# Optimization experiments

Hardware: AMD Instinct MI355X
Metric: run time of the kernel (lower is better)

Reference implementation:

```python
import jax, jax.numpy as jnp
import numpy as np
import math

DN = ('NCHW', 'OIHW', 'NCHW')

def conv(x, w, b, stride=1, pad=0):
    y = jax.lax.conv_general_dilated(x, w, (stride, stride), ((pad, pad), (pad, pad)), dimension_numbers=DN)
    return y + b[None, :, None, None]

def conv_t(x, w, b, stride=2, k=4, p=1):
    # torch ConvTranspose2d: weight (Cin, Cout, kH, kW). Equivalent fractionally-strided conv:
    w2 = jnp.transpose(w[:, :, ::-1, ::-1], (1, 0, 2, 3))  # -> (Cout, Cin, kH, kW), spatially flipped
    pp = k - 1 - p
    y = jax.lax.conv_general_dilated(x, w2, (1, 1), ((pp, pp), (pp, pp)), lhs_dilation=(stride, stride), dimension_numbers=DN)
    return y + b[None, :, None, None]

def res_stack(h, w1, b1, w2, b2):
    # w1: [L, rh, nh, 3, 3], w2: [L, nh, rh, 1, 1]
    for i in range(w1.shape[0]):
        t = conv(jax.nn.relu(h), w1[i], b1[i], 1, 1)
        t = conv(jax.nn.relu(t), w2[i], b2[i], 1, 0)
        h = h + t
    return jax.nn.relu(h)

def setup_inputs() -> dict:
    key = jax.random.key(0)
    ks = jax.random.split(key, 16)
    D, K = 64, 512
    limit = math.sqrt(3.0 / D)
    def w(k, shape, scale=0.05):
        return (jax.random.normal(k, shape, dtype=jnp.float32) * scale)
    return {
        'x': jax.random.normal(ks[0], (16, 3, 256, 256), dtype=jnp.float32),
        'enc_w0': w(ks[1], (64, 3, 4, 4)), 'enc_b0': jnp.zeros((64,), jnp.float32),
        'enc_w1': w(ks[2], (128, 64, 4, 4)), 'enc_b1': jnp.zeros((128,), jnp.float32),
        'enc_wf': w(ks[3], (128, 128, 3, 3)), 'enc_bf': jnp.zeros((128,), jnp.float32),
        'enc_res_w1': w(ks[4], (2, 32, 128, 3, 3)), 'enc_res_b1': jnp.zeros((2, 32), jnp.float32),
        'enc_res_w2': w(ks[5], (2, 128, 32, 1, 1)), 'enc_res_b2': jnp.zeros((2, 128), jnp.float32),
        'pre_w': w(ks[6], (64, 128, 1, 1)), 'pre_b': jnp.zeros((64,), jnp.float32),
        'codebook': jax.random.uniform(ks[7], (D, K), jnp.float32, -limit, limit),
        'dec_w': w(ks[8], (128, 64, 3, 3)), 'dec_b': jnp.zeros((128,), jnp.float32),
        'dec_res_w1': w(ks[9], (2, 32, 128, 3, 3)), 'dec_res_b1': jnp.zeros((2, 32), jnp.float32),
        'dec_res_w2': w(ks[10], (2, 128, 32, 1, 1)), 'dec_res_b2': jnp.zeros((2, 128), jnp.float32),
        'up_w0': w(ks[11], (128, 64, 4, 4)), 'up_b0': jnp.zeros((64,), jnp.float32),
        'up_w1': w(ks[12], (64, 3, 4, 4)), 'up_b1': jnp.zeros((3,), jnp.float32),
    }

def reference(x, enc_w0, enc_b0, enc_w1, enc_b1, enc_wf, enc_bf,
              enc_res_w1, enc_res_b1, enc_res_w2, enc_res_b2,
              pre_w, pre_b, codebook,
              dec_w, dec_b, dec_res_w1, dec_res_b1, dec_res_w2, dec_res_b2,
              up_w0, up_b0, up_w1, up_b1):
    # --- Encoder ---
    h = jax.nn.relu(conv(x, enc_w0, enc_b0, 2, 1))
    h = jax.nn.relu(conv(h, enc_w1, enc_b1, 2, 1))
    h = conv(h, enc_wf, enc_bf, 1, 1)
    h = res_stack(h, enc_res_w1, enc_res_b1, enc_res_w2, enc_res_b2)
    z = conv(h, pre_w, pre_b, 1, 0)  # [B, 64, 64, 64]
    # --- Vector quantizer (cdist + argmin + gather, straight-through) ---
    B, D, H, W = z.shape
    flat = jnp.transpose(z, (0, 2, 3, 1)).reshape(-1, D)  # [BHW, D]
    dist = (flat ** 2).sum(1, keepdims=True) - 2.0 * (flat @ codebook) + (codebook ** 2).sum(0)[None, :]
    idx = jnp.argmin(dist, axis=1)  # [BHW]
    q = codebook.T[idx].reshape(B, H, W, D).transpose(0, 3, 1, 2)
    zq = z + jax.lax.stop_gradient(q - z)  # straight-through estimator
    # --- Decoder ---
    h = conv(zq, dec_w, dec_b, 1, 1)
    h = res_stack(h, dec_res_w1, dec_res_b1, dec_res_w2, dec_res_b2)
    h = jax.nn.relu(conv_t(h, up_w0, up_b0, 2, 4, 1))
    x_recon = conv_t(h, up_w1, up_b1, 2, 4, 1)
    return x_recon
```

## Files before the change

### kernel.cpp

```cpp
#include <hip/hip_runtime.h>
#include <math.h>


#define DEV __device__ __forceinline__

DEV int rfl(int v) { return __builtin_amdgcn_readfirstlane(v); }

DEV void async_copy16(const float* g, float* l) {
  __builtin_amdgcn_global_load_lds(
      (const __attribute__((address_space(1))) void*)g,
      (__attribute__((address_space(3))) void*)l, 16, 0, 0);
}

typedef __attribute__((ext_vector_type(8))) _Float16 h16x8;
typedef __attribute__((ext_vector_type(4))) float f32x4;

DEV ushort f2h(float f) {
  _Float16 h = (_Float16)f;
  return __builtin_bit_cast(ushort, h);
}
DEV float h2f(ushort u) { return (float)__builtin_bit_cast(_Float16, u); }
DEV uint pk(ushort a, ushort b) { return (uint)a | ((uint)b << 16); }

template<int CIN, int COT>
__global__ __launch_bounds__(256) void prep_w3s(
    const float* __restrict__ w, ushort* __restrict__ wpk) {
  constexpr int nCh = CIN / 32, nM = COT / 16;
  const int t = blockIdx.x * 256 + threadIdx.x;
  if (t >= 9 * nCh * nM * 64) return;
  const int l = t & 63;
  const int m = (t >> 6) % nM;
  const int sid = t / (64 * nM);
  const int ch = sid / 9, khkw = sid % 9;
  const int co = m * 16 + (l & 15);
  const int k8 = (l >> 4) * 8;
  const int sw = (16 * l) ^ ((l & 4) ? 8 : 0);
  ushort* slab = wpk + (size_t)sid * (nM * 1024) + m * 1024;
#pragma unroll
  for (int i = 0; i < 8; i++) {
    const int ci = ch * 32 + k8 + i;
    const float v = w[((size_t)co * CIN + ci) * 9 + khkw];
    const ushort hi = f2h(v);
    slab[sw + i]       = hi;
    slab[(sw ^ 8) + i] = f2h((v - h2f(hi)) * 2048.0f);
  }
}

template<int CIN, int COT>
__global__ __launch_bounds__(256) void prep_w4s(
    const float* __restrict__ w, ushort* __restrict__ wpk) {
  const int t = blockIdx.x * 256 + threadIdx.x;
  if (t >= 16384) return;
  const int l = t & 63;
  const int m = (t >> 6) & 7;
  const int sid = t >> 9;
  const int step = sid >> 3, rr = (sid >> 2) & 1, kw = sid & 3;
  const int ch = step >> 1, h = step & 1;
  const int kh = 2 * h + rr;
  const int tap = kh * 4 + kw;
  const int co = m * 16 + (l & 15);
  const int k8 = (l >> 4) * 8;
  const int sw = (16 * l) ^ ((l & 4) ? 8 : 0);
  ushort* slab = wpk + (size_t)sid * 8192 + m * 1024;
#pragma unroll
  for (int i = 0; i < 8; i++) {
    const int ci = ch * 32 + k8 + i;
    const float v = w[((size_t)co * CIN + ci) * 16 + tap];
    const ushort hi = f2h(v);
    slab[sw + i]       = hi;
    slab[(sw ^ 8) + i] = f2h((v - h2f(hi)) * 2048.0f);
  }
}

template<int CIN, int COT>
__global__ __launch_bounds__(256) void prep_wt(
    const float* __restrict__ w, ushort* __restrict__ wpk) {
  constexpr int nCh = CIN / 32, nM = COT / 16;
  const int t = blockIdx.x * 256 + threadIdx.x;
  if (t >= 16 * nCh * nM * 64) return;
  const int l = t & 63;
  int q = t >> 6;
  const int m = q % nM;  q /= nM;
  const int ch = q % nCh; q /= nCh;
  const int kh = q >> 2, kw = q & 3;
  const int co = m * 16 + (l & 15);
  const int k8 = (l >> 4) * 8;
  ushort* o = wpk + (size_t)t * 16;
#pragma unroll
  for (int i = 0; i < 8; i++) {
    const int ci = ch * 32 + k8 + i;
    const float v = w[(((size_t)ci * COT + co) * 4 + kh) * 4 + kw];
    const ushort hi = f2h(v);
    o[i]     = hi;
    o[8 + i] = f2h((v - h2f(hi)) * 2048.0f);
  }
}

__global__ __launch_bounds__(256) void prep_cb(
    const float* __restrict__ cb, ushort* __restrict__ cbpk) {
  const int t = blockIdx.x * 256 + threadIdx.x;
  const int l = t & 63;
  const int m = (t >> 6) & 31;
  const int c = t >> 11;
  const int entry = m * 16 + (l & 15);
  ushort* o = cbpk + (size_t)t * 16;
#pragma unroll
  for (int i = 0; i < 8; i++) {
    const int d = c * 32 + (l >> 4) * 8 + i;
    const float v = cb[d * 512 + entry];
    const ushort hi = f2h(v);
    o[i]     = hi;
    o[8 + i] = f2h((v - h2f(hi)) * 2048.0f);
  }
}

__global__ __launch_bounds__(256) void cvt_cbn(
    const float* __restrict__ cb, float* __restrict__ cbn) {
  const int k = blockIdx.x * 256 + threadIdx.x;
  if (k >= 512) return;
  double s = 0.0;
  for (int d = 0; d < 64; d++) {
    const double c = (double)cb[d * 512 + k];
    s = fma(c, c, s);
  }
  cbn[k] = (float)s;
}

__global__ __launch_bounds__(256) void vq_mfma(
    const float* __restrict__ cb, const ushort* __restrict__ cbpk,
    const float* __restrict__ cbn, float* __restrict__ zq) {
  const int tid = threadIdx.x;
  const int l = tid & 63;
  const int w = rfl(tid >> 6);
  const int n = blockIdx.x >> 6, row = blockIdx.x & 63;
  float* zp = zq + (size_t)n * 262144 + row * 64;
  const int pos = w * 16 + (l & 15);

  h16x8 zh[2], zl[2];
#pragma unroll
  for (int c = 0; c < 2; c++) {
#pragma unroll
    for (int i = 0; i < 8; i++) {
      const int d = c * 32 + (l >> 4) * 8 + i;
      const float v = zp[(size_t)d * 4096 + pos];
      const _Float16 h = (_Float16)v;
      zh[c][i] = h;
      zl[c][i] = (_Float16)((v - (float)h) * 2048.0f);
    }
  }

  const float SCL = 1.0f / 2048.0f;
  float bestd = 1e30f;
  int best = 0;
  for (int grp = 0; grp < 4; grp++) {
    f32x4 aH[8], aM[8];
#pragma unroll
    for (int m = 0; m < 8; m++) {
      aH[m] = (f32x4){0.f, 0.f, 0.f, 0.f};
      aM[m] = (f32x4){0.f, 0.f, 0.f, 0.f};
    }
#pragma unroll
    for (int c = 0; c < 2; c++) {
#pragma unroll
      for (int m = 0; m < 8; m++) {
        const ushort* ap = cbpk + ((size_t)(c * 32 + grp * 8 + m) * 64 + l) * 16;
        const h16x8 ah = *(const h16x8*)ap;
        const h16x8 al = *(const h16x8*)(ap + 8);
        aH[m] = __builtin_amdgcn_mfma_f32_16x16x32_f16(ah, zh[c], aH[m], 0, 0, 0);
        aM[m] = __builtin_amdgcn_mfma_f32_16x16x32_f16(al, zh[c], aM[m], 0, 0, 0);
        aM[m] = __builtin_amdgcn_mfma_f32_16x16x32_f16(ah, zl[c], aM[m], 0, 0, 0);
      }
    }
#pragma unroll
    for (int m = 0; m < 8; m++) {
#pragma unroll
      for (int j = 0; j < 4; j++) {
        const int k = grp * 128 + m * 16 + ((l >> 4) << 2) + j;
        const float dd = aH[m][j] + aM[m][j] * SCL;
        const float dist = fmaf(-2.0f, dd, cbn[k]);
        if (dist < bestd) { bestd = dist; best = k; }
      }
    }
  }

#pragma unroll
  for (int off = 16; off <= 32; off <<= 1) {
    const float d2 = __shfl_xor(bestd, off, 64);
    const int i2 = __shfl_xor(best, off, 64);
    if (d2 < bestd || (d2 == bestd && i2 < best)) { bestd = d2; best = i2; }
  }

#pragma unroll
  for (int i = 0; i < 16; i++) {
    const int d = (l >> 4) * 16 + i;
    zp[(size_t)d * 4096 + pos] = cb[d * 512 + best];
  }
}

template<int CIN, int COT, bool RELU_OUT>
__global__ __launch_bounds__(256, 2) void conv4s2_mfma(
    const float* __restrict__ x, const ushort* __restrict__ wpk,
    const float* __restrict__ bias, float* __restrict__ y) {
  constexpr int nCh = CIN / 32, nM = COT / 16;
  constexpr int nStep = nCh * 2;
  constexpr int nTap = nStep * 8;
  __shared__ ushort act[2][2][2][66][40];
  __shared__ ushort wlds[2][8192];
  const int tid = threadIdx.x;
  const int l = tid & 63;
  const int wv = rfl(tid >> 6);
  const int ho = (blockIdx.x & 7) * 8 + (blockIdx.x >> 3);
  const int n = blockIdx.z;

  {
    uint* lp = (uint*)&act[0][0][0][0][0];
    for (int s = tid; s < 16 * 20; s += 256) {
      const int c = s / 20, w32 = s % 20;
      const int which = c & 1, rest = c >> 1;
      lp[(size_t)(rest * 66 + (which ? 65 : 0)) * 20 + w32] = 0;
    }
  }

  const float* xn = x + ((size_t)n * CIN) * 16384;

  float2 sreg[2][4][2];
  float rmask[2];
  auto LOADG = [&](int step) {
    const int ch = step >> 1, h = step & 1;
#pragma unroll
    for (int rr = 0; rr < 2; rr++) {
      const int ir = 2 * ho - 1 + 2 * h + rr;
      const bool ok = (ir >= 0) && (ir < 128);
      const int irc = ok ? ir : 0;
      rmask[rr] = ok ? 1.0f : 0.0f;
#pragma unroll
      for (int cc = 0; cc < 4; cc++) {
        const int ci0 = ch * 32 + cc * 8 + wv * 2;
        sreg[rr][cc][0] = *(const float2*)(xn + (size_t)ci0 * 16384 + irc * 128 + 2 * l);
        sreg[rr][cc][1] = *(const float2*)(xn + (size_t)(ci0 + 1) * 16384 + irc * 128 + 2 * l);
      }
    }
  };
  auto WRITE = [&]() {
    uint* base = (uint*)&act[0][0][0][0][0];
#pragma unroll
    for (int rr = 0; rr < 2; rr++) {
#pragma unroll
      for (int cc = 0; cc < 4; cc++) {
        const float e0 = sreg[rr][cc][0].x * rmask[rr], o0 = sreg[rr][cc][0].y * rmask[rr];
        const float e1 = sreg[rr][cc][1].x * rmask[rr], o1 = sreg[rr][cc][1].y * rmask[rr];
        const ushort he0 = f2h(e0), ho_0 = f2h(o0);
        const ushort he1 = f2h(e1), ho_1 = f2h(o1);
        const ushort le0 = f2h((e0 - h2f(he0)) * 2048.0f);
        const ushort lo0 = f2h((o0 - h2f(ho_0)) * 2048.0f);
        const ushort le1 = f2h((e1 - h2f(he1)) * 2048.0f);
        const ushort lo1 = f2h((o1 - h2f(ho_1)) * 2048.0f);
        const int u = cc * 4 + wv;
        const size_t sl20 = (size_t)(l + 1) * 20 + u;
        base[(size_t)((0 * 2 + rr) * 2 + 0) * 1320 + sl20] = pk(he0, he1);
        base[(size_t)((0 * 2 + rr) * 2 + 1) * 1320 + sl20] = pk(ho_0, ho_1);
        base[(size_t)((1 * 2 + rr) * 2 + 0) * 1320 + sl20] = pk(le0, le1);
        base[(size_t)((1 * 2 + rr) * 2 + 1) * 1320 + sl20] = pk(lo0, lo1);
      }
    }
  };
  auto STAGEW = [&](int t, int buf) {
    const ushort* src = wpk + (size_t)t * 8192;
    ushort* dst = &wlds[buf][0];
#pragma unroll
    for (int j = 0; j < 4; j++)
      async_copy16((const float*)(src + (j * 256 + tid) * 8),
                   (float*)(dst + (j * 256 + tid) * 8));
  };

  f32x4 accH[nM], accM[nM];
#pragma unroll
  for (int m = 0; m < nM; m++) {
    const int co = m * 16 + ((l >> 4) << 2);
    accH[m] = (f32x4){bias[co], bias[co + 1], bias[co + 2], bias[co + 3]};
    accM[m] = (f32x4){0.f, 0.f, 0.f, 0.f};
  }

  const int pb = wv * 16;
  const int sw = (16 * l) ^ ((l & 4) ? 8 : 0);
  STAGEW(0, 0);
  LOADG(0);
  int tcnt = 0;
  for (int step = 0; step < nStep; step++) {
    __syncthreads();
    WRITE();
    __syncthreads();
#pragma unroll
    for (int rr = 0; rr < 2; rr++) {
#pragma unroll
      for (int kw = 0; kw < 4; kw++) {
        if (!(rr == 0 && kw == 0)) __syncthreads();
        if (tcnt + 1 < nTap) STAGEW(tcnt + 1, (tcnt + 1) & 1);
        if (rr == 0 && kw == 0 && step + 1 < nStep) LOADG(step + 1);
        const ushort* wb = &wlds[tcnt & 1][0];
        const int eo = (kw == 0 || kw == 2) ? 1 : 0;
        const int sh = (kw == 0) ? 0 : (kw == 3) ? 2 : 1;
        const int sl = pb + (l & 15) + sh;
        const h16x8 bh = *(const h16x8*)(&act[0][rr][eo][sl][(l >> 4) * 8]);
        const h16x8 bl = *(const h16x8*)(&act[1][rr][eo][sl][(l >> 4) * 8]);
#pragma unroll
        for (int m = 0; m < nM; m++) {
          const h16x8 ah = *(const h16x8*)(wb + m * 1024 + sw);
          const h16x8 al = *(const h16x8*)(wb + m * 1024 + (sw ^ 8));
          accH[m] = __builtin_amdgcn_mfma_f32_16x16x32_f16(ah, bh, accH[m], 0, 0, 0);
          accM[m] = __builtin_amdgcn_mfma_f32_16x16x32_f16(al, bh, accM[m], 0, 0, 0);
          accM[m] = __builtin_amdgcn_mfma_f32_16x16x32_f16(ah, bl, accM[m], 0, 0, 0);
        }
        tcnt++;
      }
    }
  }

  const float SCL = 1.0f / 2048.0f;
  const int pos = pb + (l & 15);
  const int r4 = (l >> 4) << 2;
#pragma unroll
  for (int m = 0; m < nM; m++) {
    const int co = m * 16 + r4;
    float* yp = y + (((size_t)(n * COT + co)) * 64 + ho) * 64 + pos;
#pragma unroll
    for (int j = 0; j < 4; j++) {
      float v = accH[m][j] + accM[m][j] * SCL;
      if (RELU_OUT) v = fmaxf(v, 0.f);
      yp[(size_t)j * 4096] = v;
    }
  }
}

template<int CIN, int COT, bool RELU_IN>
__global__ __launch_bounds__(256, 2) void conv3_mfma(
    const float* __restrict__ x, const ushort* __restrict__ wpk,
    const float* __restrict__ bias, float* __restrict__ y) {
  constexpr int nCh = CIN / 32, nM = COT / 16;
  constexpr int nTap = nCh * 9;
  __shared__ ushort act[2][3 * 66 * 40];
  __shared__ ushort wlds[2][nM * 1024];
  const int tid = threadIdx.x;
  const int l = tid & 63;
  const int wv = rfl(tid >> 6);
  const int r = blockIdx.x;
  const int n = blockIdx.z;

  {
    uint* lp = (uint*)&act[0][0];
    for (int s = tid; s < 12 * 20; s += 256) {
      const int c = s / 20, w32 = s % 20;
      const int which = c & 1;
      const int rowrel = (c >> 1) % 3;
      const int plane  = (c >> 1) / 3;
      lp[(size_t)(plane * 198 + rowrel * 66 + (which ? 65 : 0)) * 20 + w32] = 0;
    }
  }

  const float* xn = x + ((size_t)n * CIN) * 4096;

  float sreg[3][4][2];
  auto LOADG = [&](int ch) {
#pragma unroll
    for (int rr = 0; rr < 3; rr++) {
      const int ir = r - 1 + rr;
      const bool ok = (ir >= 0) && (ir < 64);
#pragma unroll
      for (int cc = 0; cc < 4; cc++) {
        const int ci0 = ch * 32 + cc * 8 + wv * 2;
        sreg[rr][cc][0] = ok ? xn[((size_t)ci0 * 64 + ir) * 64 + l] : 0.f;
        sreg[rr][cc][1] = ok ? xn[((size_t)(ci0 + 1) * 64 + ir) * 64 + l] : 0.f;
      }
    }
  };
  auto WRITE = [&]() {
    uint* ph = (uint*)&act[0][0];
    uint* pl = (uint*)&act[1][0];
#pragma unroll
    for (int rr = 0; rr < 3; rr++) {
#pragma unroll
      for (int cc = 0; cc < 4; cc++) {
        float v0 = sreg[rr][cc][0], v1 = sreg[rr][cc][1];
        if (RELU_IN) { v0 = fmaxf(v0, 0.f); v1 = fmaxf(v1, 0.f); }
        const ushort h0 = f2h(v0), h1 = f2h(v1);
        const ushort m0 = f2h((v0 - h2f(h0)) * 2048.0f);
        const ushort m1 = f2h((v1 - h2f(h1)) * 2048.0f);
        const int idx = (rr * 66 + (l + 1)) * 20 + cc * 4 + wv;
        ph[idx] = (uint)h0 | ((uint)h1 << 16);
        pl[idx] = (uint)m0 | ((uint)m1 << 16);
      }
    }
  };
  auto STAGEW = [&](int t, int buf) {
    const ushort* src = wpk + (size_t)t * (nM * 1024);
    ushort* dst = &wlds[buf][0];
#pragma unroll
    for (int j = 0; j < nM / 2; j++)
      async_copy16((const float*)(src + (j * 256 + tid) * 8),
                   (float*)(dst + (j * 256 + tid) * 8));
  };

  f32x4 accH[nM], accM[nM];
#pragma unroll
  for (int m = 0; m < nM; m++) {
    const int co = m * 16 + ((l >> 4) << 2);
    accH[m] = (f32x4){bias[co], bias[co + 1], bias[co + 2], bias[co + 3]};
    accM[m] = (f32x4){0.f, 0.f, 0.f, 0.f};
  }

  const int pb = wv * 16;
  const int sw = (16 * l) ^ ((l & 4) ? 8 : 0);
  STAGEW(0, 0);
  LOADG(0);
  int tcnt = 0;
  for (int ch = 0; ch < nCh; ch++) {
    __syncthreads();
    WRITE();
    __syncthreads();
#pragma unroll
    for (int kh = 0; kh < 3; kh++) {
#pragma unroll
      for (int kw = 0; kw < 3; kw++) {
        if (!(kh == 0 && kw == 0)) __syncthreads();
        if (tcnt + 1 < nTap) STAGEW(tcnt + 1, (tcnt + 1) & 1);
        if (kh == 0 && kw == 0 && ch + 1 < nCh) LOADG(ch + 1);
        const ushort* wb = &wlds[tcnt & 1][0];
        const int slot = kh * 66 + pb + (l & 15) + kw;
        const h16x8 bh = *(const h16x8*)(&act[0][0] + slot * 40 + (l >> 4) * 8);
        const h16x8 bl = *(const h16x8*)(&act[1][0] + slot * 40 + (l >> 4) * 8);
#pragma unroll
        for (int m = 0; m < nM; m++) {
          const h16x8 ah = *(const h16x8*)(wb + m * 1024 + sw);
          const h16x8 al = *(const h16x8*)(wb + m * 1024 + (sw ^ 8));
          accH[m] = __builtin_amdgcn_mfma_f32_16x16x32_f16(ah, bh, accH[m], 0, 0, 0);
          accM[m] = __builtin_amdgcn_mfma_f32_16x16x32_f16(al, bh, accM[m], 0, 0, 0);
          accM[m] = __builtin_amdgcn_mfma_f32_16x16x32_f16(ah, bl, accM[m], 0, 0, 0);
        }
        tcnt++;
      }
    }
  }

  const float SCL = 1.0f / 2048.0f;
  const int pos = pb + (l & 15);
  const int r4 = (l >> 4) << 2;
#pragma unroll
  for (int m = 0; m < nM; m++) {
    const int co = m * 16 + r4;
    float* yp = y + (((size_t)(n * COT + co)) * 64 + r) * 64 + pos;
#pragma unroll
    for (int j = 0; j < 4; j++)
      yp[(size_t)j * 4096] = accH[m][j] + accM[m][j] * SCL;
  }
}

template<int CIN, int COT, bool RELU_OUT>
__global__ __launch_bounds__(256, 2) void convt_mfma(
    const float* __restrict__ x, const ushort* __restrict__ wpk,
    const float* __restrict__ bias, float* __restrict__ y) {
  constexpr int nCh = CIN / 32, nM = COT / 16;
  __shared__ ushort lds[2][2][3 * 66 * 40];
  const int tid = threadIdx.x;
  const int l = tid & 63;
  const int wv = rfl(tid >> 6);
  const int a = blockIdx.x;
  const int n = blockIdx.z;

  {
    uint* lp = (uint*)&lds[0][0][0];
    for (int s = tid; s < 24 * 20; s += 256) {
      const int slot = s / 20, w32 = s % 20;
      const int which = slot & 1;
      const int rowrel = (slot >> 1) % 3;
      const int plane  = ((slot >> 1) / 3) & 1;
      const int buf    = (slot >> 1) / 6;
      lp[(size_t)((buf * 2 + plane) * 198 + rowrel * 66 + (which ? 65 : 0)) * 20 + w32] = 0;
    }
  }

  const float* xn = x + ((size_t)n * CIN) * 4096;

  float sreg[3][4][2];
  auto LOADG = [&](int ch) {
#pragma unroll
    for (int rr = 0; rr < 3; rr++) {
      const int ir = a - 1 + rr;
      const bool ok = (ir >= 0) && (ir < 64);
#pragma unroll
      for (int cc = 0; cc < 4; cc++) {
        const int ci0 = ch * 32 + cc * 8 + wv * 2;
        sreg[rr][cc][0] = ok ? xn[((size_t)ci0 * 64 + ir) * 64 + l] : 0.f;
        sreg[rr][cc][1] = ok ? xn[((size_t)(ci0 + 1) * 64 + ir) * 64 + l] : 0.f;
      }
    }
  };
  auto WRITE = [&](int buf) {
    uint* ph = (uint*)&lds[buf][0][0];
    uint* pl = (uint*)&lds[buf][1][0];
#pragma unroll
    for (int rr = 0; rr < 3; rr++) {
#pragma unroll
      for (int cc = 0; cc < 4; cc++) {
        const float v0 = sreg[rr][cc][0], v1 = sreg[rr][cc][1];
        const ushort h0 = f2h(v0), h1 = f2h(v1);
        const ushort m0 = f2h((v0 - h2f(h0)) * 2048.0f);
        const ushort m1 = f2h((v1 - h2f(h1)) * 2048.0f);
        const int idx = (rr * 66 + (l + 1)) * 20 + cc * 4 + wv;
        ph[idx] = (uint)h0 | ((uint)h1 << 16);
        pl[idx] = (uint)m0 | ((uint)m1 << 16);
      }
    }
  };

  f32x4 aH[4][nM], aM[4][nM];
#pragma unroll
  for (int m = 0; m < nM; m++) {
    const int co = m * 16 + ((l >> 4) << 2);
    const f32x4 b4 = (f32x4){bias[co], bias[co + 1], bias[co + 2], bias[co + 3]};
#pragma unroll
    for (int o = 0; o < 4; o++) { aH[o][m] = b4; aM[o][m] = (f32x4){0.f,0.f,0.f,0.f}; }
  }

  const int pb = wv * 16;
  LOADG(0); WRITE(0);
  if (nCh > 1) LOADG(1);
  int cur = 0;

#define CT_APPLY(OIDX, KH, KW) {                                              \
    const ushort* wp_ = wpk + (((size_t)((KH) * 4 + (KW)) * nCh + ch) * nM * 64 + l) * 16; \
    _Pragma("unroll")                                                         \
    for (int m = 0; m < nM; m++) {                                            \
      const h16x8 ah = *(const h16x8*)(wp_ + (size_t)m * 1024);               \
      const h16x8 al = *(const h16x8*)(wp_ + (size_t)m * 1024 + 8);           \
      aH[OIDX][m] = __builtin_amdgcn_mfma_f32_16x16x32_f16(ah, bh, aH[OIDX][m], 0, 0, 0); \
      aM[OIDX][m] = __builtin_amdgcn_mfma_f32_16x16x32_f16(al, bh, aM[OIDX][m], 0, 0, 0); \
      aM[OIDX][m] = __builtin_amdgcn_mfma_f32_16x16x32_f16(ah, bl, aM[OIDX][m], 0, 0, 0); \
    }}
#define CT_FRAG(RR, DD)                                                       \
    const int slot = (RR) * 66 + pb + (l & 15) + 1 + (DD);                    \
    const h16x8 bh = *(const h16x8*)(base_h + slot * 40 + (l >> 4) * 8);      \
    const h16x8 bl = *(const h16x8*)(base_l + slot * 40 + (l >> 4) * 8);

  for (int ch = 0; ch < nCh; ch++) {
    __syncthreads();
    const ushort* base_h = &lds[cur][0][0];
    const ushort* base_l = &lds[cur][1][0];
    { CT_FRAG(0, -1) CT_APPLY(0, 3, 3) }
    { CT_FRAG(0,  0) CT_APPLY(0, 3, 1) CT_APPLY(1, 3, 2) }
    { CT_FRAG(0, +1) CT_APPLY(1, 3, 0) }
    { CT_FRAG(1, -1) CT_APPLY(0, 1, 3) CT_APPLY(2, 2, 3) }
    { CT_FRAG(1,  0) CT_APPLY(0, 1, 1) CT_APPLY(1, 1, 2) CT_APPLY(2, 2, 1) CT_APPLY(3, 2, 2) }
    { CT_FRAG(1, +1) CT_APPLY(1, 1, 0) CT_APPLY(3, 2, 0) }
    { CT_FRAG(2, -1) CT_APPLY(2, 0, 3) }
    { CT_FRAG(2,  0) CT_APPLY(2, 0, 1) CT_APPLY(3, 0, 2) }
    { CT_FRAG(2, +1) CT_APPLY(3, 0, 0) }
    if (ch + 1 < nCh) {
      WRITE(cur ^ 1);
      if (ch + 2 < nCh) LOADG(ch + 2);
    }
    cur ^= 1;
  }
#undef CT_APPLY
#undef CT_FRAG

  const float SCL = 1.0f / 2048.0f;
  const int b = pb + (l & 15);
  const int oh0 = 2 * a;
  const int r4 = (l >> 4) << 2;
#pragma unroll
  for (int m = 0; m < nM; m++) {
    const int co = m * 16 + r4;
#pragma unroll
    for (int j = 0; j < 4; j++) {
      float v0e = aH[0][m][j] + aM[0][m][j] * SCL;
      float v0o = aH[1][m][j] + aM[1][m][j] * SCL;
      float v1e = aH[2][m][j] + aM[2][m][j] * SCL;
      float v1o = aH[3][m][j] + aM[3][m][j] * SCL;
      if (RELU_OUT) {
        v0e = fmaxf(v0e, 0.f); v0o = fmaxf(v0o, 0.f);
        v1e = fmaxf(v1e, 0.f); v1o = fmaxf(v1o, 0.f);
      }
      float* row0 = y + (((size_t)(n * COT + co + j)) * 128 + oh0) * 128;
      ((float2*)row0)[b] = make_float2(v0e, v0o);
      ((float2*)(row0 + 128))[b] = make_float2(v1e, v1o);
    }
  }
}

template<int CIN, int COT, bool RELU_OUT, int OW>
__global__ __launch_bounds__(256) void conv4s2_row(
    const float* __restrict__ x, const float* __restrict__ w,
    const float* __restrict__ bias, float* __restrict__ y,
    int Hout, int Cout) {
  const int Win = OW * 2, Hin = Hout * 2;
  const int t = blockIdx.x * 256 + threadIdx.x;
  const int wo = t & (OW - 1);
  const int ho = rfl(t / OW);
  const int co0 = blockIdx.y * COT, n = blockIdx.z;

  float acc[COT];
#pragma unroll
  for (int u = 0; u < COT; u++) acc[u] = bias[co0 + u];

  const int iw0 = 2 * wo - 1;
  const int cA = iw0 < 0 ? 0 : iw0;
  const bool mA = iw0 >= 0;
  const int cD = (iw0 + 3 < Win) ? iw0 + 3 : Win - 1;
  const bool mD = iw0 + 3 < Win;

  for (int ci = 0; ci < CIN; ci++) {
    const float* xp = x + ((size_t)(n * CIN + ci)) * Hin * Win;
    const float* wp = w + ((size_t)(co0 * CIN + ci)) * 16;
#pragma unroll
    for (int kh = 0; kh < 4; kh++) {
      const int ih = 2 * ho - 1 + kh;
      if (ih >= 0 && ih < Hin) {
        const float* row = xp + (size_t)ih * Win;
        float x0 = row[cA];      x0 = mA ? x0 : 0.f;
        float x1 = row[iw0 + 1];
        float x2 = row[iw0 + 2];
        float x3 = row[cD];      x3 = mD ? x3 : 0.f;
#pragma unroll
        for (int u = 0; u < COT; u++) {
          const float* wr = wp + u * CIN * 16 + kh * 4;
          acc[u] = fmaf(x0, wr[0], acc[u]);
          acc[u] = fmaf(x1, wr[1], acc[u]);
          acc[u] = fmaf(x2, wr[2], acc[u]);
          acc[u] = fmaf(x3, wr[3], acc[u]);
        }
      }
    }
  }
#pragma unroll
  for (int u = 0; u < COT; u++) {
    float v = acc[u];
    if (RELU_OUT) v = fmaxf(v, 0.f);
    y[(((size_t)(n * Cout + co0 + u)) * Hout + ho) * OW + wo] = v;
  }
}

template<int CIN, int COT, bool RELU_IN, bool ACCUM, bool RELU_OUT>
__global__ __launch_bounds__(256) void conv1x1_v4(
    const float* __restrict__ x, const float* __restrict__ w,
    const float* __restrict__ bias, float* __restrict__ y,
    int HW, int Cout) {
  const int p = (blockIdx.x * 256 + threadIdx.x) * 4;
  const int co0 = blockIdx.y * COT, n = blockIdx.z;

  float4 acc[COT];
#pragma unroll
  for (int u = 0; u < COT; u++) {
    const float b = bias[co0 + u];
    acc[u] = make_float4(b, b, b, b);
  }
  for (int ci = 0; ci < CIN; ci++) {
    float4 xv = *(const float4*)&x[((size_t)(n * CIN + ci)) * HW + p];
    if (RELU_IN) {
      xv.x = fmaxf(xv.x, 0.f); xv.y = fmaxf(xv.y, 0.f);
      xv.z = fmaxf(xv.z, 0.f); xv.w = fmaxf(xv.w, 0.f);
    }
#pragma unroll
    for (int u = 0; u < COT; u++) {
      const float wv = w[(co0 + u) * CIN + ci];
      acc[u].x = fmaf(xv.x, wv, acc[u].x);
      acc[u].y = fmaf(xv.y, wv, acc[u].y);
      acc[u].z = fmaf(xv.z, wv, acc[u].z);
      acc[u].w = fmaf(xv.w, wv, acc[u].w);
    }
  }
#pragma unroll
  for (int u = 0; u < COT; u++) {
    float4* yp = (float4*)&y[((size_t)(n * Cout + co0 + u)) * HW + p];
    float4 r = acc[u];
    if (ACCUM) {
      float4 h = *yp;
      r.x += h.x; r.y += h.y; r.z += h.z; r.w += h.w;
    }
    if (RELU_OUT) {
      r.x = fmaxf(r.x, 0.f); r.y = fmaxf(r.y, 0.f);
      r.z = fmaxf(r.z, 0.f); r.w = fmaxf(r.w, 0.f);
    }
    *yp = r;
  }
}

template<int CIN, int COT, bool RELU_IN, bool RELU_OUT, int WH>
__global__ __launch_bounds__(256) void convt_row(
    const float* __restrict__ x, const float* __restrict__ w,
    const float* __restrict__ bias, float* __restrict__ y,
    int Hin, int Cout) {
  const int Hout = Hin * 2;
  const int t = blockIdx.x * 256 + threadIdx.x;
  const int a = t & (WH - 1);
  const int oh = rfl(t / WH);
  const int co0 = blockIdx.y * COT, n = blockIdx.z;

  float acc0[COT], acc1[COT];
#pragma unroll
  for (int u = 0; u < COT; u++) { acc0[u] = bias[co0 + u]; acc1[u] = bias[co0 + u]; }

  const int cm = a > 0 ? a - 1 : 0;
  const bool mm = a > 0;
  const int cp = a < WH - 1 ? a + 1 : WH - 1;
  const bool mp = a < WH - 1;

  const int kh0 = (oh + 1) & 1;
#pragma unroll
  for (int dh = 0; dh < 2; dh++) {
    const int kh = kh0 + 2 * dh;
    const int ih = (oh + 1 - kh) >> 1;
    if (ih >= 0 && ih < Hin) {
      for (int ci = 0; ci < CIN; ci++) {
        const float* row = x + (((size_t)(n * CIN + ci)) * Hin + ih) * WH;
        float x0  = row[a];
        float xm1 = row[cm];  xm1 = mm ? xm1 : 0.f;
        float xp1 = row[cp];  xp1 = mp ? xp1 : 0.f;
        if (RELU_IN) {
          x0 = fmaxf(x0, 0.f); xm1 = fmaxf(xm1, 0.f); xp1 = fmaxf(xp1, 0.f);
        }
        const float* wp = w + ((size_t)(ci * Cout + co0)) * 16 + kh * 4;
#pragma unroll
        for (int u = 0; u < COT; u++) {
          const float* wr = wp + u * 16;
          acc0[u] = fmaf(x0,  wr[1], acc0[u]);
          acc0[u] = fmaf(xm1, wr[3], acc0[u]);
          acc1[u] = fmaf(xp1, wr[0], acc1[u]);
          acc1[u] = fmaf(x0,  wr[2], acc1[u]);
        }
      }
    }
  }
#pragma unroll
  for (int u = 0; u < COT; u++) {
    float v0 = acc0[u], v1 = acc1[u];
    if (RELU_OUT) { v0 = fmaxf(v0, 0.f); v1 = fmaxf(v1, 0.f); }
    float* row = y + (((size_t)(n * Cout + co0 + u)) * Hout + oh) * (2 * WH);
    ((float2*)row)[a] = make_float2(v0, v1);
  }
}

extern "C" void kernel_launch(void* const* d_in, const int* in_sizes, int n_in,
                              void* d_out, int out_size, void* d_ws, size_t ws_size,
                              hipStream_t stream) {
  const float* x          = (const float*)d_in[0];
  const float* enc_w0     = (const float*)d_in[1];
  const float* enc_b0     = (const float*)d_in[2];
  const float* enc_w1     = (const float*)d_in[3];
  const float* enc_b1     = (const float*)d_in[4];
  const float* enc_wf     = (const float*)d_in[5];
  const float* enc_bf     = (const float*)d_in[6];
  const float* enc_res_w1 = (const float*)d_in[7];
  const float* enc_res_b1 = (const float*)d_in[8];
  const float* enc_res_w2 = (const float*)d_in[9];
  const float* enc_res_b2 = (const float*)d_in[10];
  const float* pre_w      = (const float*)d_in[11];
  const float* pre_b      = (const float*)d_in[12];
  const float* codebook   = (const float*)d_in[13];
  const float* dec_w      = (const float*)d_in[14];
  const float* dec_b      = (const float*)d_in[15];
  const float* dec_res_w1 = (const float*)d_in[16];
  const float* dec_res_b1 = (const float*)d_in[17];
  const float* dec_res_w2 = (const float*)d_in[18];
  const float* dec_res_b2 = (const float*)d_in[19];
  const float* up_w0      = (const float*)d_in[20];
  const float* up_b0      = (const float*)d_in[21];
  const float* up_w1      = (const float*)d_in[22];
  const float* up_b1      = (const float*)d_in[23];
  float* out = (float*)d_out;

  float* A = (float*)d_ws;
  float* B = A + 16777216;
  float* C = B + 8388608;
  ushort* wpkF  = (ushort*)(A + 8388608);
  ushort* wpkEa = wpkF  + 294912;
  ushort* wpkEb = wpkEa + 73728;
  ushort* wpkD  = wpkEb + 73728;
  ushort* wpkDa = wpkD  + 147456;
  ushort* wpkDb = wpkDa + 73728;
  ushort* cbpk  = wpkDb + 73728;
  float*  cbn   = (float*)(cbpk + 131072);
  ushort* wpk1  = (ushort*)C;
  ushort* wpkT  = wpk1 + 262144;

  const dim3 blk(256);
  const int N = 16;

  prep_w4s<64, 128><<<dim3(64), blk, 0, stream>>>(enc_w1, wpk1);

  conv4s2_row<3, 16, true, 128><<<dim3(64, 4, N), blk, 0, stream>>>(
      x, enc_w0, enc_b0, A, 128, 64);
  conv4s2_mfma<64, 128, true><<<dim3(64, 1, N), blk, 0, stream>>>(
      A, wpk1, enc_b1, B);

  prep_w3s<128, 128><<<dim3(72), blk, 0, stream>>>(enc_wf, wpkF);
  prep_w3s<128, 32><<<dim3(18), blk, 0, stream>>>(enc_res_w1, wpkEa);
  prep_w3s<128, 32><<<dim3(18), blk, 0, stream>>>(
      enc_res_w1 + (size_t)32 * 128 * 9, wpkEb);
  prep_w3s<64, 128><<<dim3(36), blk, 0, stream>>>(dec_w, wpkD);
  prep_w3s<128, 32><<<dim3(18), blk, 0, stream>>>(dec_res_w1, wpkDa);
  prep_w3s<128, 32><<<dim3(18), blk, 0, stream>>>(
      dec_res_w1 + (size_t)32 * 128 * 9, wpkDb);
  prep_cb<<<dim3(16), blk, 0, stream>>>(codebook, cbpk);
  cvt_cbn<<<dim3(2), blk, 0, stream>>>(codebook, cbn);

  conv3_mfma<128, 128, false><<<dim3(64, 1, N), blk, 0, stream>>>(
      B, wpkF, enc_bf, C);
  conv3_mfma<128, 32, true><<<dim3(64, 1, N), blk, 0, stream>>>(
      C, wpkEa, enc_res_b1, A);
  conv1x1_v4<32, 8, true, true, false><<<dim3(4, 16, N), blk, 0, stream>>>(
      A, enc_res_w2, enc_res_b2, C, 4096, 128);
  conv3_mfma<128, 32, true><<<dim3(64, 1, N), blk, 0, stream>>>(
      C, wpkEb, enc_res_b1 + 32, A);
  conv1x1_v4<32, 8, true, true, true><<<dim3(4, 16, N), blk, 0, stream>>>(
      A, enc_res_w2 + (size_t)128 * 32, enc_res_b2 + 128, C, 4096, 128);
  conv1x1_v4<128, 8, false, false, false><<<dim3(4, 8, N), blk, 0, stream>>>(
      C, pre_w, pre_b, A, 4096, 64);

  prep_wt<128, 64><<<dim3(64), blk, 0, stream>>>(up_w0, wpkT);

  vq_mfma<<<dim3(1024), blk, 0, stream>>>(codebook, cbpk, cbn, A);

  conv3_mfma<64, 128, false><<<dim3(64, 1, N), blk, 0, stream>>>(
      A, wpkD, dec_b, B);
  conv3_mfma<128, 32, true><<<dim3(64, 1, N), blk, 0, stream>>>(
      B, wpkDa, dec_res_b1, A);
  conv1x1_v4<32, 8, true, true, false><<<dim3(4, 16, N), blk, 0, stream>>>(
      A, dec_res_w2, dec_res_b2, B, 4096, 128);
  conv3_mfma<128, 32, true><<<dim3(64, 1, N), blk, 0, stream>>>(
      B, wpkDb, dec_res_b1 + 32, A);
  conv1x1_v4<32, 8, true, true, true><<<dim3(4, 16, N), blk, 0, stream>>>(
      A, dec_res_w2 + (size_t)128 * 32, dec_res_b2 + 128, B, 4096, 128);
  convt_mfma<128, 64, true><<<dim3(64, 1, N), blk, 0, stream>>>(
      B, wpkT, up_b0, A);
  convt_row<64, 3, false, false, 128><<<dim3(128, 1, N), blk, 0, stream>>>(
      A, up_w1, up_b1, out, 128, 3);
}
```

Before: 813.8 us.

## Stage transposed-conv weights through LDS with async double-buffered copies

The transposed-conv kernel now streams each tap's weight slab into double-buffered LDS using async global-to-LDS copies, instead of every wave reading weights straight from global memory. The weight prep kernel is changed to emit slabs in the order the taps are consumed, with a swizzled layout to reduce LDS bank conflicts. The activation buffer drops from double to single buffering to make room. The cost is a __syncthreads before every tap apply plus extra barriers around the activation write, which may serialize the MFMA work.

Measured after the change: 777.7 us. 1.05x faster.

```diff
diff --git a/kernel.cpp b/kernel.cpp
--- a/kernel.cpp
+++ b/kernel.cpp
@@ -73,26 +73,29 @@
 }
 
 template<int CIN, int COT>
-__global__ __launch_bounds__(256) void prep_wt(
+__global__ __launch_bounds__(256) void prep_wts(
     const float* __restrict__ w, ushort* __restrict__ wpk) {
   constexpr int nCh = CIN / 32, nM = COT / 16;
   const int t = blockIdx.x * 256 + threadIdx.x;
   if (t >= 16 * nCh * nM * 64) return;
   const int l = t & 63;
-  int q = t >> 6;
-  const int m = q % nM;  q /= nM;
-  const int ch = q % nCh; q /= nCh;
-  const int kh = q >> 2, kw = q & 3;
+  const int m = (t >> 6) % nM;
+  const int sid = t / (64 * nM);
+  const int ch = sid >> 4, idx = sid & 15;
+  const int ord[16] = {15, 13, 14, 12, 7, 11, 5, 6, 9, 10, 4, 8, 3, 1, 2, 0};
+  const int tap = ord[idx];
+  const int kh = tap >> 2, kw = tap & 3;
   const int co = m * 16 + (l & 15);
   const int k8 = (l >> 4) * 8;
-  ushort* o = wpk + (size_t)t * 16;
+  const int sw = (16 * l) ^ ((l & 4) ? 8 : 0);
+  ushort* slab = wpk + (size_t)sid * (nM * 1024) + m * 1024;
 #pragma unroll
   for (int i = 0; i < 8; i++) {
     const int ci = ch * 32 + k8 + i;
     const float v = w[(((size_t)ci * COT + co) * 4 + kh) * 4 + kw];
     const ushort hi = f2h(v);
-    o[i]     = hi;
-    o[8 + i] = f2h((v - h2f(hi)) * 2048.0f);
+    slab[sw + i]       = hi;
+    slab[(sw ^ 8) + i] = f2h((v - h2f(hi)) * 2048.0f);
   }
 }
 
@@ -459,7 +462,9 @@
     const float* __restrict__ x, const ushort* __restrict__ wpk,
     const float* __restrict__ bias, float* __restrict__ y) {
   constexpr int nCh = CIN / 32, nM = COT / 16;
-  __shared__ ushort lds[2][2][3 * 66 * 40];
+  constexpr int nTap = nCh * 16;
+  __shared__ ushort act[2][3 * 66 * 40];
+  __shared__ ushort wlds[2][nM * 1024];
   const int tid = threadIdx.x;
   const int l = tid & 63;
   const int wv = rfl(tid >> 6);
@@ -467,14 +472,13 @@
   const int n = blockIdx.z;
 
   {
-    uint* lp = (uint*)&lds[0][0][0];
-    for (int s = tid; s < 24 * 20; s += 256) {
-      const int slot = s / 20, w32 = s % 20;
-      const int which = slot & 1;
-      const int rowrel = (slot >> 1) % 3;
-      const int plane  = ((slot >> 1) / 3) & 1;
-      const int buf    = (slot >> 1) / 6;
-      lp[(size_t)((buf * 2 + plane) * 198 + rowrel * 66 + (which ? 65 : 0)) * 20 + w32] = 0;
+    uint* lp = (uint*)&act[0][0];
+    for (int s = tid; s < 12 * 20; s += 256) {
+      const int c = s / 20, w32 = s % 20;
+      const int which = c & 1;
+      const int rowrel = (c >> 1) % 3;
+      const int plane  = (c >> 1) / 3;
+      lp[(size_t)(plane * 198 + rowrel * 66 + (which ? 65 : 0)) * 20 + w32] = 0;
     }
   }
 
@@ -494,9 +498,9 @@
       }
     }
   };
-  auto WRITE = [&](int buf) {
-    uint* ph = (uint*)&lds[buf][0][0];
-    uint* pl = (uint*)&lds[buf][1][0];
+  auto WRITE = [&]() {
+    uint* ph = (uint*)&act[0][0];
+    uint* pl = (uint*)&act[1][0];
 #pragma unroll
     for (int rr = 0; rr < 3; rr++) {
 #pragma unroll
@@ -511,6 +515,14 @@
       }
     }
   };
+  auto STAGEW = [&](int t, int buf) {
+    const ushort* src = wpk + (size_t)t * (nM * 1024);
+    ushort* dst = &wlds[buf][0];
+#pragma unroll
+    for (int j = 0; j < nM / 2; j++)
+      async_copy16((const float*)(src + (j * 256 + tid) * 8),
+                   (float*)(dst + (j * 256 + tid) * 8));
+  };
 
   f32x4 aH[4][nM], aM[4][nM];
 #pragma unroll
@@ -522,43 +534,45 @@
   }
 
   const int pb = wv * 16;
-  LOADG(0); WRITE(0);
-  if (nCh > 1) LOADG(1);
-  int cur = 0;
-
-#define CT_APPLY(OIDX, KH, KW) {                                              \
-    const ushort* wp_ = wpk + (((size_t)((KH) * 4 + (KW)) * nCh + ch) * nM * 64 + l) * 16; \
+  const int sw = (16 * l) ^ ((l & 4) ? 8 : 0);
+  STAGEW(0, 0);
+  LOADG(0);
+  int tcnt = 0;
+
+#define CT_APPLY(OIDX) {                                                      \
+    if (!first) __syncthreads();                                              \
+    first = false;                                                            \
+    if (tcnt + 1 < nTap) STAGEW(tcnt + 1, (tcnt + 1) & 1);                    \
+    if (doLoad) { if (ch + 1 < nCh) LOADG(ch + 1); doLoad = false; }          \
+    const ushort* wb = &wlds[tcnt & 1][0];                                    \
     _Pragma("unroll")                                                         \
     for (int m = 0; m < nM; m++) {                                            \
-      const h16x8 ah = *(const h16x8*)(wp_ + (size_t)m * 1024);               \
-      const h16x8 al = *(const h16x8*)(wp_ + (size_t)m * 1024 + 8);           \
+      const h16x8 ah = *(const h16x8*)(wb + m * 1024 + sw);                   \
+      const h16x8 al = *(const h16x8*)(wb + m * 1024 + (sw ^ 8));             \
       aH[OIDX][m] = __builtin_amdgcn_mfma_f32_16x16x32_f16(ah, bh, aH[OIDX][m], 0, 0, 0); \
       aM[OIDX][m] = __builtin_amdgcn_mfma_f32_16x16x32_f16(al, bh, aM[OIDX][m], 0, 0, 0); \
       aM[OIDX][m] = __builtin_amdgcn_mfma_f32_16x16x32_f16(ah, bl, aM[OIDX][m], 0, 0, 0); \
-    }}
+    }                                                                         \
+    tcnt++; }
 #define CT_FRAG(RR, DD)                                                       \
     const int slot = (RR) * 66 + pb + (l & 15) + 1 + (DD);                    \
-    const h16x8 bh = *(const h16x8*)(base_h + slot * 40 + (l >> 4) * 8);      \
-    const h16x8 bl = *(const h16x8*)(base_l + slot * 40 + (l >> 4) * 8);
+    const h16x8 bh = *(const h16x8*)(&act[0][0] + slot * 40 + (l >> 4) * 8);  \
+    const h16x8 bl = *(const h16x8*)(&act[1][0] + slot * 40 + (l >> 4) * 8);
 
   for (int ch = 0; ch < nCh; ch++) {
     __syncthreads();
-    const ushort* base_h = &lds[cur][0][0];
-    const ushort* base_l = &lds[cur][1][0];
-    { CT_FRAG(0, -1) CT_APPLY(0, 3, 3) }
-    { CT_FRAG(0,  0) CT_APPLY(0, 3, 1) CT_APPLY(1, 3, 2) }
-    { CT_FRAG(0, +1) CT_APPLY(1, 3, 0) }
-    { CT_FRAG(1, -1) CT_APPLY(0, 1, 3) CT_APPLY(2, 2, 3) }
-    { CT_FRAG(1,  0) CT_APPLY(0, 1, 1) CT_APPLY(1, 1, 2) CT_APPLY(2, 2, 1) CT_APPLY(3, 2, 2) }
-    { CT_FRAG(1, +1) CT_APPLY(1, 1, 0) CT_APPLY(3, 2, 0) }
-    { CT_FRAG(2, -1) CT_APPLY(2, 0, 3) }
-    { CT_FRAG(2,  0) CT_APPLY(2, 0, 1) CT_APPLY(3, 0, 2) }
-    { CT_FRAG(2, +1) CT_APPLY(3, 0, 0) }
-    if (ch + 1 < nCh) {
-      WRITE(cur ^ 1);
-      if (ch + 2 < nCh) LOADG(ch + 2);
-    }
-    cur ^= 1;
+    WRITE();
+    __syncthreads();
+    bool first = true, doLoad = true;
+    { CT_FRAG(0, -1) CT_APPLY(0) }
+    { CT_FRAG(0,  0) CT_APPLY(0) CT_APPLY(1) }
+    { CT_FRAG(0, +1) CT_APPLY(1) }
+    { CT_FRAG(1, -1) CT_APPLY(0) CT_APPLY(2) }
+    { CT_FRAG(1,  0) CT_APPLY(0) CT_APPLY(1) CT_APPLY(2) CT_APPLY(3) }
+    { CT_FRAG(1, +1) CT_APPLY(1) CT_APPLY(3) }
+    { CT_FRAG(2, -1) CT_APPLY(2) }
+    { CT_FRAG(2,  0) CT_APPLY(2) CT_APPLY(3) }
+    { CT_FRAG(2, +1) CT_APPLY(3) }
   }
 #undef CT_APPLY
 #undef CT_FRAG
@@ -816,7 +830,7 @@
   conv1x1_v4<128, 8, false, false, false><<<dim3(4, 8, N), blk, 0, stream>>>(
       C, pre_w, pre_b, A, 4096, 64);
 
-  prep_wt<128, 64><<<dim3(64), blk, 0, stream>>>(up_w0, wpkT);
+  prep_wts<128, 64><<<dim3(64), blk, 0, stream>>>(up_w0, wpkT);
 
   vq_mfma<<<dim3(1024), blk, 0, stream>>>(codebook, cbpk, cbn, A);
 
```
